# Kernel optimization log

Hardware: AMD Instinct MI355X
Metric: run time of the kernel (lower is better)

The kernel has to match this reference:

```python
import jax, jax.numpy as jnp
import numpy as np

NUM_EMBEDDINGS = 1024
EMBEDDING_DIM = 64
COMMITMENT_COST = 0.25


def setup_inputs() -> dict:
    key = jax.random.key(0)
    k1, k2 = jax.random.split(key)
    inputs = jax.random.normal(k1, (32, EMBEDDING_DIM, 64, 64), dtype=jnp.float32)
    # torch init: uniform(-1/K, 1/K)
    weight = jax.random.uniform(
        k2, (NUM_EMBEDDINGS, EMBEDDING_DIM), dtype=jnp.float32,
        minval=-1.0 / NUM_EMBEDDINGS, maxval=1.0 / NUM_EMBEDDINGS)
    return {"inputs": inputs, "weight": weight}


def reference(inputs, weight):
    # NCHW -> NHWC
    x = jnp.transpose(inputs, (0, 2, 3, 1))  # [B,H,W,D]
    B, H, W, D = x.shape
    flat = x.reshape(-1, D)  # [N,D]
    # squared L2 distances to each codebook entry: [N,K]
    distances = (
        jnp.sum(flat ** 2, axis=1, keepdims=True)
        + jnp.sum(weight ** 2, axis=1)
        - 2.0 * flat @ weight.T
    )
    encoding_indices = jnp.argmin(distances, axis=1)  # [N]
    # one-hot @ weight is just a gather
    quantized = weight[encoding_indices].reshape(x.shape)  # [B,H,W,D]

    e_latent_loss = jnp.mean((jax.lax.stop_gradient(quantized) - x) ** 2)
    q_latent_loss = jnp.mean((quantized - jax.lax.stop_gradient(x)) ** 2)
    loss = q_latent_loss + COMMITMENT_COST * e_latent_loss

    # straight-through estimator
    quantized_st = x + jax.lax.stop_gradient(quantized - x)
    out = jnp.transpose(quantized_st, (0, 3, 1, 2))  # NHWC -> NCHW
    return out, loss, encoding_indices[:, None]
```

## Files before the change

### kernel.cpp

```cpp
#include <hip/hip_runtime.h>
#include <math.h>

#define N_ROWS   131072
#define DIM      64
#define KCODES   1024
#define HWSZ     4096
#define CHW      262144
#define OUT_ELEMS 8388608
#define BLOCK    512
#define HALF_T   256
#define PIX      2
#define PIXBLK   (HALF_T * PIX)
#define NBLOCKS  (N_ROWS / PIXBLK)
#define KHALF    512
#define TILE_K   256
#define TILE_PAD (TILE_K + 2)

__device__ __forceinline__ float np_sumsq64(const float* v) {
#pragma clang fp contract(off)
    float r[8];
#pragma unroll
    for (int j = 0; j < 8; ++j) r[j] = v[j] * v[j];
#pragma unroll
    for (int i = 8; i < 64; i += 8) {
#pragma unroll
        for (int j = 0; j < 8; ++j) {
            float p = v[i + j] * v[i + j];
            r[j] = r[j] + p;
        }
    }
    float s01 = r[0] + r[1];
    float s23 = r[2] + r[3];
    float s45 = r[4] + r[5];
    float s67 = r[6] + r[7];
    return (s01 + s23) + (s45 + s67);
}

__global__ __launch_bounds__(256) void vq_wsum(const float* __restrict__ w,
                                               float* __restrict__ wsum) {
    int k = blockIdx.x * blockDim.x + threadIdx.x;
    const float* wr = w + k * DIM;
    float wv[DIM];
#pragma unroll
    for (int d = 0; d < DIM; ++d) wv[d] = wr[d];
    wsum[k] = np_sumsq64(wv);
}

__device__ __forceinline__ void loadq(const float4* __restrict__ swv,
                                      int kka, int kkb, int q,
                                      float4 (&r0)[4], float4 (&r1)[4]) {
#pragma unroll
    for (int j = 0; j < 4; ++j) {
        r0[j] = swv[kka * 16 + q * 4 + j];
        r1[j] = swv[kkb * 16 + q * 4 + j];
    }
}

__device__ __forceinline__ void fma16(const float4 (&r0)[4], const float4 (&r1)[4],
                                      const float* __restrict__ x0,
                                      const float* __restrict__ x1, int db,
                                      float& c00, float& c01,
                                      float& c10, float& c11) {
#pragma unroll
    for (int j = 0; j < 4; ++j) {
        const float4 va = r0[j];
        const float4 vb = r1[j];
        const int d = db + j * 4;
        c00 = __builtin_fmaf(x0[d + 0], va.x, c00); c10 = __builtin_fmaf(x1[d + 0], va.x, c10);
        c01 = __builtin_fmaf(x0[d + 0], vb.x, c01); c11 = __builtin_fmaf(x1[d + 0], vb.x, c11);
        c00 = __builtin_fmaf(x0[d + 1], va.y, c00); c10 = __builtin_fmaf(x1[d + 1], va.y, c10);
        c01 = __builtin_fmaf(x0[d + 1], vb.y, c01); c11 = __builtin_fmaf(x1[d + 1], vb.y, c11);
        c00 = __builtin_fmaf(x0[d + 2], va.z, c00); c10 = __builtin_fmaf(x1[d + 2], va.z, c10);
        c01 = __builtin_fmaf(x0[d + 2], vb.z, c01); c11 = __builtin_fmaf(x1[d + 2], vb.z, c11);
        c00 = __builtin_fmaf(x0[d + 3], va.w, c00); c10 = __builtin_fmaf(x1[d + 3], va.w, c10);
        c01 = __builtin_fmaf(x0[d + 3], vb.w, c01); c11 = __builtin_fmaf(x1[d + 3], vb.w, c11);
    }
}

__global__ __launch_bounds__(512, 2) void vq_main(const float* __restrict__ inp,
                                                  const float* __restrict__ weight,
                                                  const float* __restrict__ wsum,
                                                  float* __restrict__ out,
                                                  float* __restrict__ idx_out,
                                                  float* __restrict__ block_loss) {
    __shared__ float sw[2][TILE_PAD * DIM];
    __shared__ float sws[2][TILE_K];
    __shared__ float cbv[2][HALF_T];
    __shared__ int   cbk[2][HALF_T];
    __shared__ float red[BLOCK / 64];

    const int tid  = threadIdx.x;
    const int half = tid >> 8;
    const int t    = tid & 255;
    const int n0   = blockIdx.x * PIXBLK + t;
    const int n1   = n0 + HALF_T;
    const int b0 = n0 >> 12, hw0 = n0 & 4095;
    const int b1 = n1 >> 12, hw1 = n1 & 4095;

    const float* xb0 = inp + (size_t)b0 * CHW + hw0;
    const float* xb1 = inp + (size_t)b1 * CHW + hw1;
    float x0[DIM], x1[DIM];
#pragma unroll
    for (int d = 0; d < DIM; ++d) x0[d] = xb0[(size_t)d * HWSZ];
#pragma unroll
    for (int d = 0; d < DIM; ++d) x1[d] = xb1[(size_t)d * HWSZ];

    const float a0 = np_sumsq64(x0);
    const float a1 = np_sumsq64(x1);

    float best0 = 3.402823466e38f, best1 = 3.402823466e38f;
    int   bk0 = 0, bk1 = 0;

    const int kbase = half * KHALF;
    const float4* swv = (const float4*)(&sw[half][0]);

    for (int tile = 0; tile < KHALF; tile += TILE_K) {
        __syncthreads();
        {
            const float4* gsrc = (const float4*)(weight + (size_t)(kbase + tile) * DIM);
            float4* ldst = (float4*)(&sw[half][0]);
#pragma unroll
            for (int i = 0; i < 16; ++i)
                ldst[i * HALF_T + t] = gsrc[i * HALF_T + t];
            sws[half][t] = wsum[kbase + tile + t];
        }
        __syncthreads();

        float4 A0[4], A1[4], B0[4], B1[4];
        loadq(swv, 0, 1, 0, A0, A1);

#pragma unroll 1
        for (int kk = 0; kk < TILE_K; kk += 2) {
            const float bsw0 = sws[half][kk];
            const float bsw1 = sws[half][kk + 1];
            float c00 = 0.f, c01 = 0.f, c10 = 0.f, c11 = 0.f;

            loadq(swv, kk, kk + 1, 1, B0, B1);
            fma16(A0, A1, x0, x1, 0,  c00, c01, c10, c11);
            loadq(swv, kk, kk + 1, 2, A0, A1);
            fma16(B0, B1, x0, x1, 16, c00, c01, c10, c11);
            loadq(swv, kk, kk + 1, 3, B0, B1);
            fma16(A0, A1, x0, x1, 32, c00, c01, c10, c11);
            loadq(swv, kk + 2, kk + 3, 0, A0, A1);
            fma16(B0, B1, x0, x1, 48, c00, c01, c10, c11);

            float dk00, dk01, dk10, dk11;
            {
#pragma clang fp contract(off)
                const float sa = a0 + bsw0;
                const float sb = a0 + bsw1;
                const float ta = a1 + bsw0;
                const float tb = a1 + bsw1;
                dk00 = sa - 2.0f * c00;
                dk01 = sb - 2.0f * c01;
                dk10 = ta - 2.0f * c10;
                dk11 = tb - 2.0f * c11;
            }
            const int k0 = kbase + tile + kk;
            if (dk00 < best0) { best0 = dk00; bk0 = k0; }
            if (dk01 < best0) { best0 = dk01; bk0 = k0 + 1; }
            if (dk10 < best1) { best1 = dk10; bk1 = k0; }
            if (dk11 < best1) { best1 = dk11; bk1 = k0 + 1; }
        }
    }

    __syncthreads();
    if (half == 0) {
        cbv[0][t] = best0; cbk[0][t] = bk0;
        cbv[1][t] = best1; cbk[1][t] = bk1;
    }
    __syncthreads();

    float ls = 0.f;
    if (half == 1) {
        const float lo0 = cbv[0][t]; const int lk0 = cbk[0][t];
        const float lo1 = cbv[1][t]; const int lk1 = cbk[1][t];
        if (!(best0 < lo0)) { best0 = lo0; bk0 = lk0; }
        if (!(best1 < lo1)) { best1 = lo1; bk1 = lk1; }

        const float* wb0 = weight + bk0 * DIM;
        const float* wb1 = weight + bk1 * DIM;
        float* ob0 = out + (size_t)b0 * CHW + hw0;
        float* ob1 = out + (size_t)b1 * CHW + hw1;
#pragma unroll
        for (int c = 0; c < DIM; ++c) {
            const float wv0 = wb0[c];
            ob0[(size_t)c * HWSZ] = wv0;
            const float d0 = wv0 - x0[c];
            ls = fmaf(d0, d0, ls);
            const float wv1 = wb1[c];
            ob1[(size_t)c * HWSZ] = wv1;
            const float d1 = wv1 - x1[c];
            ls = fmaf(d1, d1, ls);
        }
        idx_out[n0] = (float)bk0;
        idx_out[n1] = (float)bk1;
    }

#pragma unroll
    for (int off = 32; off > 0; off >>= 1) ls += __shfl_down(ls, off, 64);
    const int lane = tid & 63;
    const int wid  = tid >> 6;
    if (lane == 0) red[wid] = ls;
    __syncthreads();
    if (tid == 0) {
        float s = 0.f;
#pragma unroll
        for (int w = 0; w < BLOCK / 64; ++w) s += red[w];
        block_loss[blockIdx.x] = s;
    }
}

__global__ __launch_bounds__(256) void vq_loss_reduce(const float* __restrict__ bl,
                                                      float* __restrict__ loss_out) {
    double s = 0.0;
    for (int i = threadIdx.x; i < NBLOCKS; i += 256) s += (double)bl[i];
    __shared__ double red[4];
#pragma unroll
    for (int off = 32; off > 0; off >>= 1) s += __shfl_down(s, off, 64);
    const int lane = threadIdx.x & 63;
    const int wid  = threadIdx.x >> 6;
    if (lane == 0) red[wid] = s;
    __syncthreads();
    if (threadIdx.x == 0) {
        const double total = (red[0] + red[1]) + (red[2] + red[3]);
        loss_out[0] = (float)(1.25 * total / (double)OUT_ELEMS);
    }
}

extern "C" void kernel_launch(void* const* d_in, const int* in_sizes, int n_in,
                              void* d_out, int out_size, void* d_ws, size_t ws_size,
                              hipStream_t stream) {
    const float* inp    = (const float*)d_in[0];
    const float* weight = (const float*)d_in[1];

    float* out_q    = (float*)d_out;
    float* out_loss = (float*)d_out + OUT_ELEMS;
    float* out_idx  = (float*)d_out + OUT_ELEMS + 1;

    float* wsum       = (float*)d_ws;
    float* block_loss = (float*)d_ws + KCODES;

    vq_wsum<<<KCODES / 256, 256, 0, stream>>>(weight, wsum);
    vq_main<<<NBLOCKS, BLOCK, 0, stream>>>(inp, weight, wsum,
                                           out_q, out_idx, block_loss);
    vq_loss_reduce<<<1, BLOCK / 2, 0, stream>>>(block_loss, out_loss);
}
```

Before: 313.6 us.

## Split codebook operand between LDS and uniform global loads to halve LDS traffic

Only the first 32 dimensions of each codebook tile are staged in shared memory. The remaining 32 dimensions are read straight from global memory through a pointer laundered via shared memory, so the compiler treats it as wave-uniform and can emit scalar loads. The aim is to halve LDS bandwidth and footprint in the inner distance loop by moving part of the operand traffic onto the scalar/constant cache path. The risk is global-load latency in a loop unrolled only once, with no explicit prefetch, and the earlier software pipelining of LDS loads is removed.

```diff
diff --git a/kernel.cpp b/kernel.cpp
--- a/kernel.cpp
+++ b/kernel.cpp
@@ -14,7 +14,6 @@
 #define NBLOCKS  (N_ROWS / PIXBLK)
 #define KHALF    512
 #define TILE_K   256
-#define TILE_PAD (TILE_K + 2)
 
 __device__ __forceinline__ float np_sumsq64(const float* v) {
 #pragma clang fp contract(off)
@@ -44,16 +43,6 @@
 #pragma unroll
     for (int d = 0; d < DIM; ++d) wv[d] = wr[d];
     wsum[k] = np_sumsq64(wv);
-}
-
-__device__ __forceinline__ void loadq(const float4* __restrict__ swv,
-                                      int kka, int kkb, int q,
-                                      float4 (&r0)[4], float4 (&r1)[4]) {
-#pragma unroll
-    for (int j = 0; j < 4; ++j) {
-        r0[j] = swv[kka * 16 + q * 4 + j];
-        r1[j] = swv[kkb * 16 + q * 4 + j];
-    }
 }
 
 __device__ __forceinline__ void fma16(const float4 (&r0)[4], const float4 (&r1)[4],
@@ -83,11 +72,12 @@
                                                   float* __restrict__ out,
                                                   float* __restrict__ idx_out,
                                                   float* __restrict__ block_loss) {
-    __shared__ float sw[2][TILE_PAD * DIM];
+    __shared__ float sw[2][TILE_K * 32];
     __shared__ float sws[2][TILE_K];
     __shared__ float cbv[2][HALF_T];
     __shared__ int   cbk[2][HALF_T];
     __shared__ float red[BLOCK / 64];
+    __shared__ unsigned long long wop;
 
     const int tid  = threadIdx.x;
     const int half = tid >> 8;
@@ -97,6 +87,8 @@
     const int b0 = n0 >> 12, hw0 = n0 & 4095;
     const int b1 = n1 >> 12, hw1 = n1 & 4095;
 
+    if (tid == 0) wop = (unsigned long long)(uintptr_t)weight;
+
     const float* xb0 = inp + (size_t)b0 * CHW + hw0;
     const float* xb1 = inp + (size_t)b1 * CHW + hw1;
     float x0[DIM], x1[DIM];
@@ -112,7 +104,9 @@
     int   bk0 = 0, bk1 = 0;
 
     const int kbase = half * KHALF;
-    const float4* swv = (const float4*)(&sw[half][0]);
+
+    __syncthreads();
+    const float* wmem = (const float*)(uintptr_t)wop;
 
     for (int tile = 0; tile < KHALF; tile += TILE_K) {
         __syncthreads();
@@ -120,29 +114,53 @@
             const float4* gsrc = (const float4*)(weight + (size_t)(kbase + tile) * DIM);
             float4* ldst = (float4*)(&sw[half][0]);
 #pragma unroll
-            for (int i = 0; i < 16; ++i)
-                ldst[i * HALF_T + t] = gsrc[i * HALF_T + t];
+            for (int i = 0; i < 8; ++i) {
+                const int idx = i * HALF_T + t;
+                ldst[idx] = gsrc[((idx >> 3) << 4) | (idx & 7)];
+            }
             sws[half][t] = wsum[kbase + tile + t];
         }
         __syncthreads();
 
-        float4 A0[4], A1[4], B0[4], B1[4];
-        loadq(swv, 0, 1, 0, A0, A1);
+        const float4* swv = (const float4*)(&sw[half][0]);
+        const float4* u0p = (const float4*)wmem + ((size_t)(kbase + tile) << 4) + 8;
+        const float4* u1p = u0p + 16;
 
 #pragma unroll 1
         for (int kk = 0; kk < TILE_K; kk += 2) {
+            float4 U20[4], U30[4], U21[4], U31[4];
+#pragma unroll
+            for (int j = 0; j < 4; ++j) {
+                U20[j] = u0p[j];
+                U30[j] = u0p[4 + j];
+                U21[j] = u1p[j];
+                U31[j] = u1p[4 + j];
+            }
+
             const float bsw0 = sws[half][kk];
             const float bsw1 = sws[half][kk + 1];
             float c00 = 0.f, c01 = 0.f, c10 = 0.f, c11 = 0.f;
 
-            loadq(swv, kk, kk + 1, 1, B0, B1);
-            fma16(A0, A1, x0, x1, 0,  c00, c01, c10, c11);
-            loadq(swv, kk, kk + 1, 2, A0, A1);
-            fma16(B0, B1, x0, x1, 16, c00, c01, c10, c11);
-            loadq(swv, kk, kk + 1, 3, B0, B1);
-            fma16(A0, A1, x0, x1, 32, c00, c01, c10, c11);
-            loadq(swv, kk + 2, kk + 3, 0, A0, A1);
-            fma16(B0, B1, x0, x1, 48, c00, c01, c10, c11);
+            {
+                float4 L0[4], L1[4];
+#pragma unroll
+                for (int j = 0; j < 4; ++j) {
+                    L0[j] = swv[kk * 8 + j];
+                    L1[j] = swv[(kk + 1) * 8 + j];
+                }
+                fma16(L0, L1, x0, x1, 0, c00, c01, c10, c11);
+            }
+            {
+                float4 L0[4], L1[4];
+#pragma unroll
+                for (int j = 0; j < 4; ++j) {
+                    L0[j] = swv[kk * 8 + 4 + j];
+                    L1[j] = swv[(kk + 1) * 8 + 4 + j];
+                }
+                fma16(L0, L1, x0, x1, 16, c00, c01, c10, c11);
+            }
+            fma16(U20, U21, x0, x1, 32, c00, c01, c10, c11);
+            fma16(U30, U31, x0, x1, 48, c00, c01, c10, c11);
 
             float dk00, dk01, dk10, dk11;
             {
@@ -161,6 +179,8 @@
             if (dk01 < best0) { best0 = dk01; bk0 = k0 + 1; }
             if (dk10 < best1) { best1 = dk10; bk1 = k0; }
             if (dk11 < best1) { best1 = dk11; bk1 = k0 + 1; }
+
+            u0p += 32; u1p += 32;
         }
     }
 
@@ -244,5 +264,5 @@
     vq_wsum<<<KCODES / 256, 256, 0, stream>>>(weight, wsum);
     vq_main<<<NBLOCKS, BLOCK, 0, stream>>>(inp, weight, wsum,
                                            out_q, out_idx, block_loss);
-    vq_loss_reduce<<<1, BLOCK / 2, 0, stream>>>(block_loss, out_loss);
-}
+    vq_loss_reduce<<<1, 256, 0, stream>>>(block_loss, out_loss);
+}
```

Result: slower. 349.9 us (+11.6%).
